# Kernel optimization log

Hardware: AMD Instinct MI355X
Metric: run time of the kernel (lower is better)

Reference implementation:

```python
import jax, jax.numpy as jnp
import numpy as np

B, S, H, M, E = 64, 512, 1024, 26, 676  # batch, seq, hidden, max_nodes, max_edges (M*M)


def setup_inputs() -> dict:
    key = jax.random.key(0)
    ks = jax.random.split(key, 16)
    seq = jax.random.normal(ks[0], (B, S, H), jnp.float32)
    # ragged, strictly-increasing sentence-end offsets in [1, S-1], zero-padded tail
    rng = np.random.RandomState(0)
    off = np.zeros((B, M - 1), np.int64)
    for b in range(B):
        c = rng.randint(5, M)  # count of valid offsets per sample (ragged)
        off[b, :c] = np.sort(rng.choice(np.arange(1, S), size=c, replace=False))
    s = 1.0 / np.sqrt(H)
    s3 = 1.0 / np.sqrt(3 * H)
    return {
        'sequence_outputs': seq,
        'proof_offsets': jnp.asarray(off),
        'node_labels': jax.random.randint(ks[1], (B, M), 0, 2),
        'edge_labels': jax.random.randint(ks[2], (B, E), 0, 2),
        'W_naf': jax.random.normal(ks[3], (H, H), jnp.float32) * s,
        'b_naf': jnp.zeros((H,), jnp.float32),
        'W_cd': jax.random.normal(ks[4], (H, H), jnp.float32) * s,
        'b_cd': jnp.zeros((H,), jnp.float32),
        'W_co': jax.random.normal(ks[5], (H, 2), jnp.float32) * s,
        'b_co': jnp.zeros((2,), jnp.float32),
        'W_nd': jax.random.normal(ks[6], (H, H), jnp.float32) * s,
        'b_nd': jnp.zeros((H,), jnp.float32),
        'W_no': jax.random.normal(ks[7], (H, 2), jnp.float32) * s,
        'b_no': jnp.zeros((2,), jnp.float32),
        'W_ed': jax.random.normal(ks[8], (3 * H, H), jnp.float32) * s3,
        'b_ed': jnp.zeros((H,), jnp.float32),
        'W_eo': jax.random.normal(ks[9], (H, 2), jnp.float32) * s,
        'b_eo': jnp.zeros((2,), jnp.float32),
    }


def reference(sequence_outputs, proof_offsets, node_labels, edge_labels,
              W_naf, b_naf, W_cd, b_cd, W_co, b_co,
              W_nd, b_nd, W_no, b_no, W_ed, b_ed, W_eo, b_eo):
    Bx, Sx, Hx = sequence_outputs.shape
    Mx = node_labels.shape[1]
    Ex = edge_labels.shape[1]

    cls = sequence_outputs[:, 0, :]                       # [B,H]
    naf = cls @ W_naf + b_naf                             # NAF node embedding
    logits = jnp.tanh(cls @ W_cd + b_cd) @ W_co + b_co    # RobertaClassificationHead (eval: dropout=id)

    # segment-mean pooling via inclusive prefix sums: segment j = tokens (prev_j, off_j]
    P = jnp.cumsum(sequence_outputs, axis=1)              # [B,S,H]
    off = proof_offsets                                   # [B,M-1]
    prev = jnp.concatenate([jnp.zeros((Bx, 1), off.dtype), off[:, :-1]], axis=1)
    valid = off > 0                                       # [B,M-1]
    seg_sum = (jnp.take_along_axis(P, off[..., None], axis=1)
               - jnp.take_along_axis(P, prev[..., None], axis=1))  # [B,M-1,H]
    seg_len = jnp.maximum(off - prev, 1).astype(sequence_outputs.dtype)
    seg_mean = seg_sum / seg_len[..., None] * valid[..., None]

    count = valid.sum(axis=1)                             # nodes per sample (excl. NAF)
    # node embeddings: seg means at 0..count-1, NAF at index count, zeros after
    node_full = jnp.concatenate([seg_mean, jnp.zeros((Bx, 1, Hx), seg_mean.dtype)], axis=1)  # [B,M,H]
    idx = jnp.arange(Mx)
    node_full = node_full + (idx[None, :, None] == count[:, None, None]) * naf[:, None, :]

    # all-pairs edge features over n=count+1 nodes, row-major flat k=i*n+j, zero-padded to E
    n = count + 1                                         # [B]
    k = jnp.arange(Ex)                                    # [E]
    i = jnp.clip(k[None, :] // n[:, None], 0, Mx - 1)     # [B,E]
    j = jnp.clip(k[None, :] % n[:, None], 0, Mx - 1)
    valid_e = (k[None, :] < (n * n)[:, None])[..., None]
    ni = jnp.take_along_axis(node_full, i[..., None], axis=1)  # [B,E,H]
    nj = jnp.take_along_axis(node_full, j[..., None], axis=1)
    edge = jnp.concatenate([nj, ni, nj - ni], axis=-1) * valid_e  # [B,E,3H]

    node_logits = jnp.tanh(node_full @ W_nd + b_nd) @ W_no + b_no
    edge_logits = jnp.tanh(edge @ W_ed + b_ed) @ W_eo + b_eo
    return (logits, node_logits, edge_logits)
```

## Files before the change

kernel.cpp:

```cpp
#include <hip/hip_runtime.h>
#include <hip/hip_bf16.h>

#define B_ 64
#define S_ 512
#define H_ 1024
#define M_ 26
#define E_ 676

typedef short bf16x8 __attribute__((ext_vector_type(8)));
typedef float f32x4 __attribute__((ext_vector_type(4)));

__device__ __forceinline__ void gload16(const void* g, void* l) {
    __builtin_amdgcn_global_load_lds((const __attribute__((address_space(1))) unsigned int*)g,
                                     (__attribute__((address_space(3))) unsigned int*)l,
                                     16, 0, 0);
}

__device__ __forceinline__ float tanh_fast(float x) {
    float e = __expf(2.0f * x);
    return 1.0f - 2.0f * __builtin_amdgcn_rcpf(e + 1.0f);
}

__global__ __launch_bounds__(256) void k_seg(
    const float* __restrict__ seq, const int* __restrict__ off,
    float* __restrict__ node_sum) {
    __shared__ float buf[4][16 * 256];
    __shared__ int offs_s[32];
    int bid = blockIdx.x;
    int tid = threadIdx.x;
    int b = bid >> 2, hs = bid & 3;
    int w = tid >> 6;
    int lane4 = (tid & 63) * 4;

    if (tid < M_ - 1) offs_s[tid] = off[b * (M_ - 1) + tid];
    __syncthreads();

    int c = 0;
    while (c < M_ - 1 && offs_s[c] > 0) c++;
    int offmax = offs_s[c - 1];
    int nt = (offmax + 15) >> 4;

    float* ns_base = node_sum + ((size_t)b * M_) * H_ + hs * 256 + tid;
    for (int m = c; m < M_; ++m) ns_base[(size_t)m * H_] = 0.f;

    const float* src0 = seq + (size_t)b * S_ * H_ + hs * 256;
#pragma unroll
    for (int j0 = 0; j0 < 4; ++j0) {
#pragma unroll
        for (int i = 0; i < 4; ++i) {
            int r = 4 * w + i;
            int t = 1 + 16 * j0 + r; t = min(t, 511);
            gload16(src0 + (size_t)t * H_ + lane4, &buf[j0][r * 256]);
        }
    }

    int m = 0;
    int cur = offs_s[0];
    float acc = 0.f;
    int ntc = (nt > 4) ? nt : 4;
    for (int j = 0; j < nt; ++j) {
        int ahead = ntc - 1 - j; ahead = (ahead > 3) ? 3 : ahead;
        if (ahead == 3)      asm volatile("s_waitcnt vmcnt(12)" ::: "memory");
        else if (ahead == 2) asm volatile("s_waitcnt vmcnt(8)" ::: "memory");
        else if (ahead == 1) asm volatile("s_waitcnt vmcnt(4)" ::: "memory");
        else                 asm volatile("s_waitcnt vmcnt(0)" ::: "memory");
        __builtin_amdgcn_s_barrier();

        const float* bj = &buf[j & 3][0];
        int tbase = 1 + 16 * j;
        if (tbase + 15 <= offmax) {
#pragma unroll
            for (int r = 0; r < 16; ++r) {
                int t = tbase + r;
                acc += bj[r * 256 + tid];
                if (t == cur) {
                    ns_base[(size_t)m * H_] = acc;
                    acc = 0.f; ++m;
                    cur = (m < c) ? offs_s[m] : 0x7fffffff;
                }
            }
        } else {
            for (int r = 0; r < 16; ++r) {
                int t = tbase + r;
                if (t > offmax) break;
                acc += bj[r * 256 + tid];
                if (t == cur) {
                    ns_base[(size_t)m * H_] = acc;
                    acc = 0.f; ++m;
                    cur = (m < c) ? offs_s[m] : 0x7fffffff;
                }
            }
        }
        __builtin_amdgcn_s_barrier();
        if (j + 4 < nt) {
#pragma unroll
            for (int i = 0; i < 4; ++i) {
                int r = 4 * w + i;
                int t = 1 + 16 * (j + 4) + r; t = min(t, 511);
                gload16(src0 + (size_t)t * H_ + lane4, &buf[j & 3][r * 256]);
            }
        }
    }
    asm volatile("s_waitcnt vmcnt(0)" ::: "memory");
}

__global__ __launch_bounds__(256) void k_stage1b(
    const float* __restrict__ seq, const int* __restrict__ off,
    const float* __restrict__ Wnaf, const float* __restrict__ Wcd,
    const float* __restrict__ Wnd, const float* __restrict__ Wed,
    const float* __restrict__ bed, const float* __restrict__ Weo,
    const float* __restrict__ beo,
    __hip_bfloat16* __restrict__ Wt, int* __restrict__ count,
    float* __restrict__ econ, float* __restrict__ naf, float* __restrict__ cdh) {
    __shared__ float smem[2048];
    int bid = blockIdx.x;
    int tid = threadIdx.x;

    if (bid < 256) {
        float (*As)[64] = (float(*)[64])smem;
        float (*Bs)[64] = (float(*)[64])(smem + 1024);
        int e = bid;
        int bx = e & 31;
        int kbase = (e >> 5) * 128;
        const float* W;
        float* dst;
        int cbase;
        if (bx < 16) { W = Wnaf; dst = naf; cbase = bx * 64; }
        else         { W = Wcd;  dst = cdh; cbase = (bx - 16) * 64; }
        int tx = tid % 16, ty = tid / 16;
        float c[4][4] = {};
        int la_row = tid / 4;
        int la_k4  = (tid % 4) * 4;
        int lb_k   = tid / 16;
        int lb_c4  = (tid % 16) * 4;
        for (int k0 = 0; k0 < 128; k0 += 16) {
            float4 a = *(const float4*)(seq + (size_t)la_row * S_ * H_ + kbase + k0 + la_k4);
            *(float4*)(&Bs[lb_k][lb_c4]) =
                *(const float4*)(W + (size_t)(kbase + k0 + lb_k) * H_ + cbase + lb_c4);
            As[la_k4 + 0][la_row] = a.x;
            As[la_k4 + 1][la_row] = a.y;
            As[la_k4 + 2][la_row] = a.z;
            As[la_k4 + 3][la_row] = a.w;
            __syncthreads();
#pragma unroll
            for (int kk = 0; kk < 16; ++kk) {
                float4 av = *(const float4*)(&As[kk][ty * 4]);
                float4 bv = *(const float4*)(&Bs[kk][tx * 4]);
                c[0][0] += av.x * bv.x; c[0][1] += av.x * bv.y; c[0][2] += av.x * bv.z; c[0][3] += av.x * bv.w;
                c[1][0] += av.y * bv.x; c[1][1] += av.y * bv.y; c[1][2] += av.y * bv.z; c[1][3] += av.y * bv.w;
                c[2][0] += av.z * bv.x; c[2][1] += av.z * bv.y; c[2][2] += av.z * bv.z; c[2][3] += av.z * bv.w;
                c[3][0] += av.w * bv.x; c[3][1] += av.w * bv.y; c[3][2] += av.w * bv.z; c[3][3] += av.w * bv.w;
            }
            __syncthreads();
        }
#pragma unroll
        for (int i = 0; i < 4; ++i)
#pragma unroll
            for (int j = 0; j < 4; ++j)
                atomicAdd(dst + (size_t)(ty * 4 + i) * H_ + cbase + tx * 4 + j, c[i][j]);
    } else if (bid < 3328) {
        float (*T)[33] = (float(*)[33])smem;
        int idx = bid - 256;
        int s = idx >> 10, rem = idx & 1023;
        int bx = rem & 31, by = rem >> 5;
        int c = tid & 31, r0 = tid >> 5;
        const int HH = H_ * H_;
#pragma unroll
        for (int i = 0; i < 4; ++i) {
            int r = r0 + 8 * i;
            size_t k = by * 32 + r, n = bx * 32 + c;
            float v;
            if (s == 0)      v = Wnd[k * H_ + n];
            else if (s == 1) v = Wed[k * H_ + n] + Wed[2 * HH + k * H_ + n];
            else             v = Wed[HH + k * H_ + n] - Wed[2 * HH + k * H_ + n];
            T[r][c] = v;
        }
        __syncthreads();
#pragma unroll
        for (int i = 0; i < 4; ++i) {
            int rr = r0 + 8 * i;
            Wt[(size_t)(s * H_ + bx * 32 + rr) * H_ + by * 32 + c] = __float2bfloat16(T[c][rr]);
        }
    } else if (bid == 3328) {
        if (tid < 64) {
            int b = tid;
            int c = 0;
            for (int m = 0; m < M_ - 1; ++m) c += (off[b * (M_ - 1) + m] > 0) ? 1 : 0;
            count[b] = c;
        }
    } else {
        float* s0 = smem; float* s1 = smem + 256;
        float a0 = 0.f, a1 = 0.f;
        for (int h = tid; h < H_; h += 256) {
            float t = tanh_fast(bed[h]);
            a0 += t * Weo[h * 2 + 0];
            a1 += t * Weo[h * 2 + 1];
        }
        s0[tid] = a0; s1[tid] = a1; __syncthreads();
        for (int o = 128; o > 0; o >>= 1) {
            if (tid < o) { s0[tid] += s0[tid + o]; s1[tid] += s1[tid + o]; }
            __syncthreads();
        }
        if (tid == 0) { econ[0] = s0[0] + beo[0]; econ[1] = s1[0] + beo[1]; }
    }
}

__global__ __launch_bounds__(256) void k_stage2(
    const float* __restrict__ sums, const int* __restrict__ off,
    const int* __restrict__ count, const float* __restrict__ naf,
    const float* __restrict__ bnaf, __hip_bfloat16* __restrict__ nodeB,
    const float* __restrict__ cdh, const float* __restrict__ bcd,
    const float* __restrict__ Wco, const float* __restrict__ bco,
    float* __restrict__ out) {
    __shared__ float smem[512];
    int bid = blockIdx.x;
    int tid = threadIdx.x;
    if (bid < 1664) {
        int b = bid / 26, m = bid - b * 26;
        int cnt = count[b];
        float4 v = make_float4(0, 0, 0, 0);
        const float4* row = (const float4*)(sums + ((size_t)(b * M_ + m)) * H_);
        if (m < M_ - 1) {
            int o = off[b * (M_ - 1) + m];
            if (o > 0) {
                int prev = (m > 0) ? off[b * (M_ - 1) + m - 1] : 0;
                float inv = 1.0f / (float)max(o - prev, 1);
                float4 s = row[tid];
                v = make_float4(s.x * inv, s.y * inv, s.z * inv, s.w * inv);
            }
        }
        if (m == cnt) {
            float4 a = ((const float4*)(naf + (size_t)b * H_))[tid];
            float4 bb = ((const float4*)bnaf)[tid];
            v.x += a.x + bb.x; v.y += a.y + bb.y; v.z += a.z + bb.z; v.w += a.w + bb.w;
        }
        __hip_bfloat16 __attribute__((aligned(8))) h[4] = {
            __float2bfloat16(v.x), __float2bfloat16(v.y),
            __float2bfloat16(v.z), __float2bfloat16(v.w)};
        *(ushort4*)(nodeB + ((size_t)(b * M_ + m)) * H_ + tid * 4) = *(const ushort4*)h;
    } else {
        int b = bid - 1664;
        float* s0 = smem; float* s1 = smem + 256;
        float a0 = 0.f, a1 = 0.f;
        for (int h = tid; h < H_; h += 256) {
            float t = tanh_fast(cdh[(size_t)b * H_ + h] + bcd[h]);
            a0 += t * Wco[h * 2 + 0];
            a1 += t * Wco[h * 2 + 1];
        }
        s0[tid] = a0; s1[tid] = a1; __syncthreads();
        for (int o = 128; o > 0; o >>= 1) {
            if (tid < o) { s0[tid] += s0[tid + o]; s1[tid] += s1[tid + o]; }
            __syncthreads();
        }
        if (tid == 0) { out[b * 2 + 0] = s0[0] + bco[0]; out[b * 2 + 1] = s1[0] + bco[1]; }
    }
}

#define GM 1664
#define GN 3072
#define GK 1024
__global__ __launch_bounds__(256) void k_mfma(const __hip_bfloat16* __restrict__ A,
                                              const __hip_bfloat16* __restrict__ Bt,
                                              float* __restrict__ C) {
    __shared__ __hip_bfloat16 As[128 * 32];
    __shared__ __hip_bfloat16 Bs[128 * 32];
    int tid = threadIdx.x;
    int wid = tid >> 6, ln = tid & 63;
    int row0 = blockIdx.y * 128, col0 = blockIdx.x * 128;
    const __hip_bfloat16* ga = A + (size_t)(row0 + wid * 16 + (ln >> 2)) * GK + (ln & 3) * 8;
    const __hip_bfloat16* gb = Bt + (size_t)(col0 + wid * 16 + (ln >> 2)) * GK + (ln & 3) * 8;
    __hip_bfloat16* lA = As + wid * 512;
    __hip_bfloat16* lB = Bs + wid * 512;
    int mrow = (wid >> 1) * 64, ncol = (wid & 1) * 64;
    int l15 = ln & 15, l4 = ln >> 4;
    f32x4 acc[4][4] = {};
    const __hip_bfloat16* pa = As + (size_t)(mrow + l15) * 32 + l4 * 8;
    const __hip_bfloat16* pb = Bs + (size_t)(ncol + l15) * 32 + l4 * 8;
    for (int k0 = 0; k0 < GK; k0 += 32) {
        gload16(ga, lA);
        gload16(ga + 64 * GK, lA + 2048);
        gload16(gb, lB);
        gload16(gb + 64 * GK, lB + 2048);
        ga += 32; gb += 32;
        __syncthreads();
        bf16x8 af[4], bf[4];
#pragma unroll
        for (int mi = 0; mi < 4; ++mi) af[mi] = *(const bf16x8*)(pa + mi * 16 * 32);
#pragma unroll
        for (int ni = 0; ni < 4; ++ni) bf[ni] = *(const bf16x8*)(pb + ni * 16 * 32);
#pragma unroll
        for (int mi = 0; mi < 4; ++mi)
#pragma unroll
            for (int ni = 0; ni < 4; ++ni)
                acc[mi][ni] = __builtin_amdgcn_mfma_f32_16x16x32_bf16(af[mi], bf[ni],
                                                                      acc[mi][ni], 0, 0, 0);
        __syncthreads();
    }
#pragma unroll
    for (int mi = 0; mi < 4; ++mi)
#pragma unroll
        for (int ni = 0; ni < 4; ++ni) {
            f32x4 v = acc[mi][ni];
            size_t r = row0 + mrow + mi * 16 + l4 * 4;
            size_t cc = col0 + ncol + ni * 16 + l15;
            C[(r + 0) * GN + cc] = v[0];
            C[(r + 1) * GN + cc] = v[1];
            C[(r + 2) * GN + cc] = v[2];
            C[(r + 3) * GN + cc] = v[3];
        }
}

__global__ __launch_bounds__(256) void k_stage4(
    const float* __restrict__ Cm, const int* __restrict__ count,
    const float* __restrict__ bnd, const float* __restrict__ Wno,
    const float* __restrict__ bno, const float* __restrict__ bed,
    const float* __restrict__ Weo, const float* __restrict__ beo,
    const float* __restrict__ econ, float* __restrict__ out_n,
    float* __restrict__ out_e) {
    int bid = blockIdx.x;
    int wid = threadIdx.x >> 6, lane = threadIdx.x & 63;
    if (bid < 416) {
        int r = bid * 4 + wid;
        const float4* src = (const float4*)(Cm + (size_t)r * GN);
        float a0 = 0.f, a1 = 0.f;
#pragma unroll
        for (int it = 0; it < 4; ++it) {
            int h = lane * 4 + it * 256;
            float4 s = src[lane + it * 64];
            float4 bb = *(const float4*)(bnd + h);
            float t0 = tanh_fast(s.x + bb.x), t1 = tanh_fast(s.y + bb.y);
            float t2 = tanh_fast(s.z + bb.z), t3 = tanh_fast(s.w + bb.w);
            a0 += t0 * Wno[h * 2 + 0] + t1 * Wno[h * 2 + 2] + t2 * Wno[h * 2 + 4] + t3 * Wno[h * 2 + 6];
            a1 += t0 * Wno[h * 2 + 1] + t1 * Wno[h * 2 + 3] + t2 * Wno[h * 2 + 5] + t3 * Wno[h * 2 + 7];
        }
        for (int o = 32; o > 0; o >>= 1) { a0 += __shfl_down(a0, o); a1 += __shfl_down(a1, o); }
        if (lane == 0) { out_n[(size_t)r * 2 + 0] = a0 + bno[0]; out_n[(size_t)r * 2 + 1] = a1 + bno[1]; }
    } else {
        int e = bid - 416;
        int b = e >> 4;
        int wg = (e & 15) * 4 + wid;
        int n = count[b] + 1;
        int n2 = n * n;
        float4 bed4[4], w04[4], w14[4];
#pragma unroll
        for (int it = 0; it < 4; ++it) {
            int h = lane * 4 + it * 256;
            bed4[it] = *(const float4*)(bed + h);
            w04[it] = make_float4(Weo[h * 2 + 0], Weo[h * 2 + 2], Weo[h * 2 + 4], Weo[h * 2 + 6]);
            w14[it] = make_float4(Weo[h * 2 + 1], Weo[h * 2 + 3], Weo[h * 2 + 5], Weo[h * 2 + 7]);
        }
        float e0 = econ[0], e1 = econ[1];
        float b0 = beo[0], b1 = beo[1];
        for (int k = wg; k < E_; k += 64) {
            float* dst = out_e + ((size_t)b * E_ + k) * 2;
            if (k >= n2) {
                if (lane == 0) { dst[0] = e0; dst[1] = e1; }
                continue;
            }
            int i = k / n, j = k - i * n;
            const float4* U4 = (const float4*)(Cm + (size_t)(b * M_ + j) * GN + H_);
            const float4* V4 = (const float4*)(Cm + (size_t)(b * M_ + i) * GN + 2 * H_);
            float a0 = 0.f, a1 = 0.f;
#pragma unroll
            for (int it = 0; it < 4; ++it) {
                float4 u = U4[lane + it * 64];
                float4 v = V4[lane + it * 64];
                float t0 = tanh_fast(u.x + v.x + bed4[it].x);
                float t1 = tanh_fast(u.y + v.y + bed4[it].y);
                float t2 = tanh_fast(u.z + v.z + bed4[it].z);
                float t3 = tanh_fast(u.w + v.w + bed4[it].w);
                a0 += t0 * w04[it].x + t1 * w04[it].y + t2 * w04[it].z + t3 * w04[it].w;
                a1 += t0 * w14[it].x + t1 * w14[it].y + t2 * w14[it].z + t3 * w14[it].w;
            }
            for (int o = 32; o > 0; o >>= 1) { a0 += __shfl_down(a0, o); a1 += __shfl_down(a1, o); }
            if (lane == 0) { dst[0] = a0 + b0; dst[1] = a1 + b1; }
        }
    }
}

extern "C" void kernel_launch(void* const* d_in, const int* in_sizes, int n_in,
                              void* d_out, int out_size, void* d_ws, size_t ws_size,
                              hipStream_t stream) {
    const float* seq  = (const float*)d_in[0];
    const int*   off  = (const int*)d_in[1];
    const float* Wnaf = (const float*)d_in[4];  const float* bnaf = (const float*)d_in[5];
    const float* Wcd  = (const float*)d_in[6];  const float* bcd  = (const float*)d_in[7];
    const float* Wco  = (const float*)d_in[8];  const float* bco  = (const float*)d_in[9];
    const float* Wnd  = (const float*)d_in[10]; const float* bnd  = (const float*)d_in[11];
    const float* Wno  = (const float*)d_in[12]; const float* bno  = (const float*)d_in[13];
    const float* Wed  = (const float*)d_in[14]; const float* bed  = (const float*)d_in[15];
    const float* Weo  = (const float*)d_in[16]; const float* beo  = (const float*)d_in[17];
    float* out = (float*)d_out;

    float* ws = (float*)d_ws;
    size_t p = 0;
    float* nodeS = ws + p;  p += (size_t)B_ * M_ * H_;
    float* naf   = ws + p;  p += (size_t)B_ * H_;
    float* cdh   = ws + p;  p += (size_t)B_ * H_;
    __hip_bfloat16* nodeB = (__hip_bfloat16*)(ws + p); p += (size_t)B_ * M_ * H_ / 2;
    __hip_bfloat16* Wt    = (__hip_bfloat16*)(ws + p); p += (size_t)3 * H_ * H_ / 2;
    float* Cbuf  = ws + p;  p += (size_t)B_ * M_ * 3 * H_;
    int*   cnt   = (int*)(ws + p); p += 64;
    float* econ  = ws + p;  p += 2;

    hipMemsetAsync(naf, 0, 2 * (size_t)B_ * H_ * sizeof(float), stream);

    k_seg<<<dim3(256), 256, 0, stream>>>(seq, off, nodeS);
    k_stage1b<<<dim3(3330), 256, 0, stream>>>(seq, off, Wnaf, Wcd, Wnd, Wed, bed, Weo, beo,
                                              Wt, cnt, econ, naf, cdh);
    k_stage2<<<dim3(1728), 256, 0, stream>>>(nodeS, off, cnt, naf, bnaf, nodeB,
                                             cdh, bcd, Wco, bco, out);
    k_mfma<<<dim3(GN / 128, GM / 128), 256, 0, stream>>>(nodeB, Wt, Cbuf);
    k_stage4<<<dim3(1440), 256, 0, stream>>>(Cbuf, cnt, bnd, Wno, bno, bed, Weo, beo, econ,
                                             out + B_ * 2, out + B_ * 2 + B_ * M_ * 2);
}
```

Measured before the change: 327.4 us.

## Fuse segment-mean bf16 output, node-head epilogue into GEMM, deepen prefetch

The segment-sum kernel now divides by segment length and writes bf16 node embeddings directly, so the fp32 node-sum buffer and most of the stage-2 normalization pass go away. The GEMM epilogue for the node-projection columns applies tanh and the 2-wide output projection in registers, reducing with shuffles and atomics, so only the edge columns of C are stored. The weight-transpose work is packed into fewer blocks that each process 12 tiles with software prefetch, and the sequence prefetch ring grows from 4 to 6 stages. This cuts global traffic and launch work, but adds atomics in the GEMM epilogue and uses more LDS in the segment kernel.

```diff
diff --git a/kernel.cpp b/kernel.cpp
--- a/kernel.cpp
+++ b/kernel.cpp
@@ -23,8 +23,8 @@
 
 __global__ __launch_bounds__(256) void k_seg(
     const float* __restrict__ seq, const int* __restrict__ off,
-    float* __restrict__ node_sum) {
-    __shared__ float buf[4][16 * 256];
+    __hip_bfloat16* __restrict__ nodeB) {
+    __shared__ float buf[6][16 * 256];
     __shared__ int offs_s[32];
     int bid = blockIdx.x;
     int tid = threadIdx.x;
@@ -39,69 +39,84 @@
     while (c < M_ - 1 && offs_s[c] > 0) c++;
     int offmax = offs_s[c - 1];
     int nt = (offmax + 15) >> 4;
-
-    float* ns_base = node_sum + ((size_t)b * M_) * H_ + hs * 256 + tid;
-    for (int m = c; m < M_; ++m) ns_base[(size_t)m * H_] = 0.f;
+    int ntc = (nt > 6) ? nt : 6;
+
+    __hip_bfloat16* nb = nodeB + ((size_t)b * M_) * H_ + hs * 256 + tid;
+    for (int m = c; m < M_; ++m) nb[(size_t)m * H_] = __float2bfloat16(0.f);
 
     const float* src0 = seq + (size_t)b * S_ * H_ + hs * 256;
 #pragma unroll
-    for (int j0 = 0; j0 < 4; ++j0) {
+    for (int j0 = 0; j0 < 6; ++j0)
 #pragma unroll
         for (int i = 0; i < 4; ++i) {
-            int r = 4 * w + i;
-            int t = 1 + 16 * j0 + r; t = min(t, 511);
-            gload16(src0 + (size_t)t * H_ + lane4, &buf[j0][r * 256]);
-        }
-    }
+            int t = 1 + 16 * j0 + 4 * w + i; t = min(t, 511);
+            gload16(src0 + (size_t)t * H_ + lane4, &buf[j0][(4 * w + i) * 256]);
+        }
 
     int m = 0;
     int cur = offs_s[0];
+    int prevoff = 0;
     float acc = 0.f;
-    int ntc = (nt > 4) ? nt : 4;
+    int slot = 0;
     for (int j = 0; j < nt; ++j) {
-        int ahead = ntc - 1 - j; ahead = (ahead > 3) ? 3 : ahead;
-        if (ahead == 3)      asm volatile("s_waitcnt vmcnt(12)" ::: "memory");
-        else if (ahead == 2) asm volatile("s_waitcnt vmcnt(8)" ::: "memory");
-        else if (ahead == 1) asm volatile("s_waitcnt vmcnt(4)" ::: "memory");
-        else                 asm volatile("s_waitcnt vmcnt(0)" ::: "memory");
+        int ahead = ntc - 1 - j; if (ahead > 5) ahead = 5;
+        switch (ahead) {
+            case 5:  asm volatile("s_waitcnt vmcnt(20)" ::: "memory"); break;
+            case 4:  asm volatile("s_waitcnt vmcnt(16)" ::: "memory"); break;
+            case 3:  asm volatile("s_waitcnt vmcnt(12)" ::: "memory"); break;
+            case 2:  asm volatile("s_waitcnt vmcnt(8)" ::: "memory"); break;
+            case 1:  asm volatile("s_waitcnt vmcnt(4)" ::: "memory"); break;
+            default: asm volatile("s_waitcnt vmcnt(0)" ::: "memory"); break;
+        }
         __builtin_amdgcn_s_barrier();
 
-        const float* bj = &buf[j & 3][0];
+        const float* bj = &buf[slot][0];
+        float vals[16];
+#pragma unroll
+        for (int r = 0; r < 16; ++r) vals[r] = bj[r * 256 + tid];
+
         int tbase = 1 + 16 * j;
-        if (tbase + 15 <= offmax) {
-#pragma unroll
-            for (int r = 0; r < 16; ++r) {
+        int rmax = offmax - tbase; if (rmax > 15) rmax = 15;
+#pragma unroll
+        for (int r = 0; r < 16; ++r) {
+            if (r <= rmax) {
+                acc += vals[r];
                 int t = tbase + r;
-                acc += bj[r * 256 + tid];
                 if (t == cur) {
-                    ns_base[(size_t)m * H_] = acc;
-                    acc = 0.f; ++m;
+                    float inv = 1.0f / (float)(cur - prevoff);
+                    nb[(size_t)m * H_] = __float2bfloat16(acc * inv);
+                    acc = 0.f; prevoff = cur; ++m;
                     cur = (m < c) ? offs_s[m] : 0x7fffffff;
                 }
             }
-        } else {
-            for (int r = 0; r < 16; ++r) {
-                int t = tbase + r;
-                if (t > offmax) break;
-                acc += bj[r * 256 + tid];
-                if (t == cur) {
-                    ns_base[(size_t)m * H_] = acc;
-                    acc = 0.f; ++m;
-                    cur = (m < c) ? offs_s[m] : 0x7fffffff;
-                }
-            }
         }
         __builtin_amdgcn_s_barrier();
-        if (j + 4 < nt) {
+        if (j + 6 < ntc) {
 #pragma unroll
             for (int i = 0; i < 4; ++i) {
-                int r = 4 * w + i;
-                int t = 1 + 16 * (j + 4) + r; t = min(t, 511);
-                gload16(src0 + (size_t)t * H_ + lane4, &buf[j & 3][r * 256]);
-            }
-        }
+                int t = 1 + 16 * (j + 6) + 4 * w + i; t = min(t, 511);
+                gload16(src0 + (size_t)t * H_ + lane4, &buf[slot][(4 * w + i) * 256]);
+            }
+        }
+        slot = (slot == 5) ? 0 : slot + 1;
     }
     asm volatile("s_waitcnt vmcnt(0)" ::: "memory");
+}
+
+__device__ __forceinline__ void load_tile(int idx, int c, int r0,
+                                          const float* __restrict__ Wnd,
+                                          const float* __restrict__ Wed, float* v) {
+    const int HH = H_ * H_;
+    int s = idx >> 10, rem = idx & 1023;
+    int bx = rem & 31, by = rem >> 5;
+#pragma unroll
+    for (int i = 0; i < 4; ++i) {
+        int r = r0 + 8 * i;
+        size_t k = (size_t)(by * 32 + r), n = (size_t)(bx * 32 + c);
+        if (s == 0)      v[i] = Wnd[k * H_ + n];
+        else if (s == 1) v[i] = Wed[k * H_ + n] + Wed[2 * HH + k * H_ + n];
+        else             v[i] = Wed[HH + k * H_ + n] - Wed[2 * HH + k * H_ + n];
+    }
 }
 
 __global__ __launch_bounds__(256) void k_stage1b(
@@ -119,9 +134,8 @@
     if (bid < 256) {
         float (*As)[64] = (float(*)[64])smem;
         float (*Bs)[64] = (float(*)[64])(smem + 1024);
-        int e = bid;
-        int bx = e & 31;
-        int kbase = (e >> 5) * 128;
+        int bx = bid & 31;
+        int kbase = (bid >> 5) * 128;
         const float* W;
         float* dst;
         int cbase;
@@ -158,30 +172,35 @@
 #pragma unroll
             for (int j = 0; j < 4; ++j)
                 atomicAdd(dst + (size_t)(ty * 4 + i) * H_ + cbase + tx * 4 + j, c[i][j]);
-    } else if (bid < 3328) {
+    } else if (bid < 512) {
         float (*T)[33] = (float(*)[33])smem;
-        int idx = bid - 256;
-        int s = idx >> 10, rem = idx & 1023;
-        int bx = rem & 31, by = rem >> 5;
         int c = tid & 31, r0 = tid >> 5;
-        const int HH = H_ * H_;
-#pragma unroll
-        for (int i = 0; i < 4; ++i) {
-            int r = r0 + 8 * i;
-            size_t k = by * 32 + r, n = bx * 32 + c;
-            float v;
-            if (s == 0)      v = Wnd[k * H_ + n];
-            else if (s == 1) v = Wed[k * H_ + n] + Wed[2 * HH + k * H_ + n];
-            else             v = Wed[HH + k * H_ + n] - Wed[2 * HH + k * H_ + n];
-            T[r][c] = v;
-        }
-        __syncthreads();
-#pragma unroll
-        for (int i = 0; i < 4; ++i) {
-            int rr = r0 + 8 * i;
-            Wt[(size_t)(s * H_ + bx * 32 + rr) * H_ + by * 32 + c] = __float2bfloat16(T[c][rr]);
-        }
-    } else if (bid == 3328) {
+        int base = (bid - 256) * 12;
+        float cur[4], nxt[4];
+        load_tile(base, c, r0, Wnd, Wed, cur);
+        for (int q = 0; q < 12; ++q) {
+            if (q < 11) load_tile(base + q + 1, c, r0, Wnd, Wed, nxt);
+            int idx = base + q;
+            int s = idx >> 10, rem = idx & 1023;
+            int bx = rem & 31, by = rem >> 5;
+#pragma unroll
+            for (int i = 0; i < 4; ++i) T[r0 + 8 * i][c] = cur[i];
+            asm volatile("s_waitcnt lgkmcnt(0)" ::: "memory");
+            __builtin_amdgcn_s_barrier();
+#pragma unroll
+            for (int i = 0; i < 4; ++i) {
+                int rr = r0 + 8 * i;
+                Wt[(size_t)(s * H_ + bx * 32 + rr) * H_ + by * 32 + c] =
+                    __float2bfloat16(T[c][rr]);
+            }
+            asm volatile("s_waitcnt lgkmcnt(0)" ::: "memory");
+            __builtin_amdgcn_s_barrier();
+            if (q < 11) {
+#pragma unroll
+                for (int i = 0; i < 4; ++i) cur[i] = nxt[i];
+            }
+        }
+    } else if (bid == 512) {
         if (tid < 64) {
             int b = tid;
             int c = 0;
@@ -205,41 +224,25 @@
     }
 }
 
-__global__ __launch_bounds__(256) void k_stage2(
-    const float* __restrict__ sums, const int* __restrict__ off,
-    const int* __restrict__ count, const float* __restrict__ naf,
-    const float* __restrict__ bnaf, __hip_bfloat16* __restrict__ nodeB,
+__global__ __launch_bounds__(256) void k_stage2s(
+    const float* __restrict__ naf, const float* __restrict__ bnaf,
+    const int* __restrict__ count, __hip_bfloat16* __restrict__ nodeB,
     const float* __restrict__ cdh, const float* __restrict__ bcd,
     const float* __restrict__ Wco, const float* __restrict__ bco,
     float* __restrict__ out) {
     __shared__ float smem[512];
     int bid = blockIdx.x;
     int tid = threadIdx.x;
-    if (bid < 1664) {
-        int b = bid / 26, m = bid - b * 26;
-        int cnt = count[b];
-        float4 v = make_float4(0, 0, 0, 0);
-        const float4* row = (const float4*)(sums + ((size_t)(b * M_ + m)) * H_);
-        if (m < M_ - 1) {
-            int o = off[b * (M_ - 1) + m];
-            if (o > 0) {
-                int prev = (m > 0) ? off[b * (M_ - 1) + m - 1] : 0;
-                float inv = 1.0f / (float)max(o - prev, 1);
-                float4 s = row[tid];
-                v = make_float4(s.x * inv, s.y * inv, s.z * inv, s.w * inv);
-            }
-        }
-        if (m == cnt) {
-            float4 a = ((const float4*)(naf + (size_t)b * H_))[tid];
-            float4 bb = ((const float4*)bnaf)[tid];
-            v.x += a.x + bb.x; v.y += a.y + bb.y; v.z += a.z + bb.z; v.w += a.w + bb.w;
-        }
+    if (bid < 64) {
+        int b = bid, cnt = count[b];
+        float4 a = ((const float4*)(naf + (size_t)b * H_))[tid];
+        float4 bb = ((const float4*)bnaf)[tid];
         __hip_bfloat16 __attribute__((aligned(8))) h[4] = {
-            __float2bfloat16(v.x), __float2bfloat16(v.y),
-            __float2bfloat16(v.z), __float2bfloat16(v.w)};
-        *(ushort4*)(nodeB + ((size_t)(b * M_ + m)) * H_ + tid * 4) = *(const ushort4*)h;
+            __float2bfloat16(a.x + bb.x), __float2bfloat16(a.y + bb.y),
+            __float2bfloat16(a.z + bb.z), __float2bfloat16(a.w + bb.w)};
+        *(ushort4*)(nodeB + ((size_t)(b * M_ + cnt)) * H_ + tid * 4) = *(const ushort4*)h;
     } else {
-        int b = bid - 1664;
+        int b = bid - 64;
         float* s0 = smem; float* s1 = smem + 256;
         float a0 = 0.f, a1 = 0.f;
         for (int h = tid; h < H_; h += 256) {
@@ -259,9 +262,13 @@
 #define GM 1664
 #define GN 3072
 #define GK 1024
+#define CB_N 2048
 __global__ __launch_bounds__(256) void k_mfma(const __hip_bfloat16* __restrict__ A,
                                               const __hip_bfloat16* __restrict__ Bt,
-                                              float* __restrict__ C) {
+                                              float* __restrict__ C,
+                                              const float* __restrict__ bnd,
+                                              const float* __restrict__ Wno,
+                                              float* __restrict__ nacc) {
     __shared__ __hip_bfloat16 As[128 * 32];
     __shared__ __hip_bfloat16 Bs[128 * 32];
     int tid = threadIdx.x;
@@ -296,49 +303,63 @@
                                                                       acc[mi][ni], 0, 0, 0);
         __syncthreads();
     }
-#pragma unroll
-    for (int mi = 0; mi < 4; ++mi)
+    if (col0 >= 1024) {
+#pragma unroll
+        for (int mi = 0; mi < 4; ++mi)
+#pragma unroll
+            for (int ni = 0; ni < 4; ++ni) {
+                f32x4 v = acc[mi][ni];
+                size_t r = row0 + mrow + mi * 16 + l4 * 4;
+                size_t cc = col0 + ncol + ni * 16 + l15 - 1024;
+                C[(r + 0) * CB_N + cc] = v[0];
+                C[(r + 1) * CB_N + cc] = v[1];
+                C[(r + 2) * CB_N + cc] = v[2];
+                C[(r + 3) * CB_N + cc] = v[3];
+            }
+    } else {
+        float bndv[4], w0v[4], w1v[4];
 #pragma unroll
         for (int ni = 0; ni < 4; ++ni) {
-            f32x4 v = acc[mi][ni];
-            size_t r = row0 + mrow + mi * 16 + l4 * 4;
-            size_t cc = col0 + ncol + ni * 16 + l15;
-            C[(r + 0) * GN + cc] = v[0];
-            C[(r + 1) * GN + cc] = v[1];
-            C[(r + 2) * GN + cc] = v[2];
-            C[(r + 3) * GN + cc] = v[3];
-        }
+            int col = col0 + ncol + ni * 16 + l15;
+            bndv[ni] = bnd[col];
+            w0v[ni] = Wno[2 * col];
+            w1v[ni] = Wno[2 * col + 1];
+        }
+#pragma unroll
+        for (int mi = 0; mi < 4; ++mi)
+#pragma unroll
+            for (int jj = 0; jj < 4; ++jj) {
+                float s0 = 0.f, s1 = 0.f;
+#pragma unroll
+                for (int ni = 0; ni < 4; ++ni) {
+                    float t = tanh_fast(acc[mi][ni][jj] + bndv[ni]);
+                    s0 += t * w0v[ni];
+                    s1 += t * w1v[ni];
+                }
+                s0 += __shfl_xor(s0, 1, 16); s0 += __shfl_xor(s0, 2, 16);
+                s0 += __shfl_xor(s0, 4, 16); s0 += __shfl_xor(s0, 8, 16);
+                s1 += __shfl_xor(s1, 1, 16); s1 += __shfl_xor(s1, 2, 16);
+                s1 += __shfl_xor(s1, 4, 16); s1 += __shfl_xor(s1, 8, 16);
+                if (l15 == 0) {
+                    int r = row0 + mrow + mi * 16 + l4 * 4 + jj;
+                    atomicAdd(nacc + 2 * r + 0, s0);
+                    atomicAdd(nacc + 2 * r + 1, s1);
+                }
+            }
+    }
 }
 
 __global__ __launch_bounds__(256) void k_stage4(
     const float* __restrict__ Cm, const int* __restrict__ count,
-    const float* __restrict__ bnd, const float* __restrict__ Wno,
-    const float* __restrict__ bno, const float* __restrict__ bed,
-    const float* __restrict__ Weo, const float* __restrict__ beo,
-    const float* __restrict__ econ, float* __restrict__ out_n,
-    float* __restrict__ out_e) {
+    const float* __restrict__ nacc, const float* __restrict__ bno,
+    const float* __restrict__ bed, const float* __restrict__ Weo,
+    const float* __restrict__ beo, const float* __restrict__ econ,
+    float* __restrict__ out_n, float* __restrict__ out_e) {
     int bid = blockIdx.x;
     int wid = threadIdx.x >> 6, lane = threadIdx.x & 63;
-    if (bid < 416) {
-        int r = bid * 4 + wid;
-        const float4* src = (const float4*)(Cm + (size_t)r * GN);
-        float a0 = 0.f, a1 = 0.f;
-#pragma unroll
-        for (int it = 0; it < 4; ++it) {
-            int h = lane * 4 + it * 256;
-            float4 s = src[lane + it * 64];
-            float4 bb = *(const float4*)(bnd + h);
-            float t0 = tanh_fast(s.x + bb.x), t1 = tanh_fast(s.y + bb.y);
-            float t2 = tanh_fast(s.z + bb.z), t3 = tanh_fast(s.w + bb.w);
-            a0 += t0 * Wno[h * 2 + 0] + t1 * Wno[h * 2 + 2] + t2 * Wno[h * 2 + 4] + t3 * Wno[h * 2 + 6];
-            a1 += t0 * Wno[h * 2 + 1] + t1 * Wno[h * 2 + 3] + t2 * Wno[h * 2 + 5] + t3 * Wno[h * 2 + 7];
-        }
-        for (int o = 32; o > 0; o >>= 1) { a0 += __shfl_down(a0, o); a1 += __shfl_down(a1, o); }
-        if (lane == 0) { out_n[(size_t)r * 2 + 0] = a0 + bno[0]; out_n[(size_t)r * 2 + 1] = a1 + bno[1]; }
-    } else {
-        int e = bid - 416;
-        int b = e >> 4;
-        int wg = (e & 15) * 4 + wid;
+    if (bid < 1024) {
+        int b = bid >> 4;
+        int wg = (bid & 15) * 4 + wid;
         int n = count[b] + 1;
         int n2 = n * n;
         float4 bed4[4], w04[4], w14[4];
@@ -358,8 +379,8 @@
                 continue;
             }
             int i = k / n, j = k - i * n;
-            const float4* U4 = (const float4*)(Cm + (size_t)(b * M_ + j) * GN + H_);
-            const float4* V4 = (const float4*)(Cm + (size_t)(b * M_ + i) * GN + 2 * H_);
+            const float4* U4 = (const float4*)(Cm + (size_t)(b * M_ + j) * CB_N);
+            const float4* V4 = (const float4*)(Cm + (size_t)(b * M_ + i) * CB_N + 1024);
             float a0 = 0.f, a1 = 0.f;
 #pragma unroll
             for (int it = 0; it < 4; ++it) {
@@ -375,6 +396,9 @@
             for (int o = 32; o > 0; o >>= 1) { a0 += __shfl_down(a0, o); a1 += __shfl_down(a1, o); }
             if (lane == 0) { dst[0] = a0 + b0; dst[1] = a1 + b1; }
         }
+    } else {
+        for (int idx = threadIdx.x; idx < GM * 2; idx += 256)
+            out_n[idx] = nacc[idx] + bno[idx & 1];
     }
 }
 
@@ -394,23 +418,23 @@
 
     float* ws = (float*)d_ws;
     size_t p = 0;
-    float* nodeS = ws + p;  p += (size_t)B_ * M_ * H_;
     float* naf   = ws + p;  p += (size_t)B_ * H_;
     float* cdh   = ws + p;  p += (size_t)B_ * H_;
+    float* nacc  = ws + p;  p += (size_t)GM * 2;
     __hip_bfloat16* nodeB = (__hip_bfloat16*)(ws + p); p += (size_t)B_ * M_ * H_ / 2;
     __hip_bfloat16* Wt    = (__hip_bfloat16*)(ws + p); p += (size_t)3 * H_ * H_ / 2;
-    float* Cbuf  = ws + p;  p += (size_t)B_ * M_ * 3 * H_;
+    float* Cbuf  = ws + p;  p += (size_t)GM * CB_N;
     int*   cnt   = (int*)(ws + p); p += 64;
     float* econ  = ws + p;  p += 2;
 
-    hipMemsetAsync(naf, 0, 2 * (size_t)B_ * H_ * sizeof(float), stream);
-
-    k_seg<<<dim3(256), 256, 0, stream>>>(seq, off, nodeS);
-    k_stage1b<<<dim3(3330), 256, 0, stream>>>(seq, off, Wnaf, Wcd, Wnd, Wed, bed, Weo, beo,
-                                              Wt, cnt, econ, naf, cdh);
-    k_stage2<<<dim3(1728), 256, 0, stream>>>(nodeS, off, cnt, naf, bnaf, nodeB,
+    hipMemsetAsync(naf, 0, (2 * (size_t)B_ * H_ + GM * 2) * sizeof(float), stream);
+
+    k_seg<<<dim3(256), 256, 0, stream>>>(seq, off, nodeB);
+    k_stage1b<<<dim3(514), 256, 0, stream>>>(seq, off, Wnaf, Wcd, Wnd, Wed, bed, Weo, beo,
+                                             Wt, cnt, econ, naf, cdh);
+    k_stage2s<<<dim3(128), 256, 0, stream>>>(naf, bnaf, cnt, nodeB,
                                              cdh, bcd, Wco, bco, out);
-    k_mfma<<<dim3(GN / 128, GM / 128), 256, 0, stream>>>(nodeB, Wt, Cbuf);
-    k_stage4<<<dim3(1440), 256, 0, stream>>>(Cbuf, cnt, bnd, Wno, bno, bed, Weo, beo, econ,
+    k_mfma<<<dim3(GN / 128, GM / 128), 256, 0, stream>>>(nodeB, Wt, Cbuf, bnd, Wno, nacc);
+    k_stage4<<<dim3(1025), 256, 0, stream>>>(Cbuf, cnt, nacc, bno, bed, Weo, beo, econ,
                                              out + B_ * 2, out + B_ * 2 + B_ * M_ * 2);
 }
```

Result: slower. 344.9 us (+5.3%).

## Compute segment means as bf16 MFMA selection-matrix matmul writing bf16 nodes directly

Applied to the files above, without the earlier changes.

Replaces the serial per-thread scan in the segment-sum kernel with a matmul: a 0/1 selection matrix in LDS times bf16-converted sequence tiles, computed with MFMA and scaled by each segment's inverse length. The result goes straight to bf16 node embeddings, so the fp32 node-sum buffer and most of stage2's per-node normalisation blocks go away. Stage2 now only writes the NAF row and computes the classifier head. The risk is that converting inputs to bf16 before summing loses precision, and the register-staged loads with a full vmcnt wait may expose memory latency.

```diff
diff --git a/kernel.cpp b/kernel.cpp
--- a/kernel.cpp
+++ b/kernel.cpp
@@ -21,87 +21,117 @@
     return 1.0f - 2.0f * __builtin_amdgcn_rcpf(e + 1.0f);
 }
 
-__global__ __launch_bounds__(256) void k_seg(
+__global__ __launch_bounds__(256) void k_segmm(
     const float* __restrict__ seq, const int* __restrict__ off,
-    float* __restrict__ node_sum) {
-    __shared__ float buf[4][16 * 256];
-    __shared__ int offs_s[32];
+    __hip_bfloat16* __restrict__ nodeB) {
+    __shared__ __hip_bfloat16 selL[32][520];
+    __shared__ __hip_bfloat16 ldsB[2][256][40];
+    __shared__ int offs_s[28];
+    __shared__ float invL[32];
+    int tid = threadIdx.x;
     int bid = blockIdx.x;
-    int tid = threadIdx.x;
-    int b = bid >> 2, hs = bid & 3;
-    int w = tid >> 6;
-    int lane4 = (tid & 63) * 4;
+    int b = bid >> 2, h0 = (bid & 3) * 256;
+    int w = tid >> 6, l = tid & 63;
 
     if (tid < M_ - 1) offs_s[tid] = off[b * (M_ - 1) + tid];
     __syncthreads();
-
     int c = 0;
     while (c < M_ - 1 && offs_s[c] > 0) c++;
     int offmax = offs_s[c - 1];
-    int nt = (offmax + 15) >> 4;
-
-    float* ns_base = node_sum + ((size_t)b * M_) * H_ + hs * 256 + tid;
-    for (int m = c; m < M_; ++m) ns_base[(size_t)m * H_] = 0.f;
-
-    const float* src0 = seq + (size_t)b * S_ * H_ + hs * 256;
-#pragma unroll
-    for (int j0 = 0; j0 < 4; ++j0) {
-#pragma unroll
-        for (int i = 0; i < 4; ++i) {
-            int r = 4 * w + i;
-            int t = 1 + 16 * j0 + r; t = min(t, 511);
-            gload16(src0 + (size_t)t * H_ + lane4, &buf[j0][r * 256]);
-        }
-    }
-
-    int m = 0;
-    int cur = offs_s[0];
-    float acc = 0.f;
-    int ntc = (nt > 4) ? nt : 4;
-    for (int j = 0; j < nt; ++j) {
-        int ahead = ntc - 1 - j; ahead = (ahead > 3) ? 3 : ahead;
-        if (ahead == 3)      asm volatile("s_waitcnt vmcnt(12)" ::: "memory");
-        else if (ahead == 2) asm volatile("s_waitcnt vmcnt(8)" ::: "memory");
-        else if (ahead == 1) asm volatile("s_waitcnt vmcnt(4)" ::: "memory");
-        else                 asm volatile("s_waitcnt vmcnt(0)" ::: "memory");
+
+    {
+        unsigned* p = (unsigned*)&selL[0][0];
+        const int tot = 32 * 520 * 2 / 4;
+        for (int i = tid; i < tot; i += 256) p[i] = 0u;
+    }
+    if (tid < 32)
+        invL[tid] = (tid < c) ? 1.0f / (float)(offs_s[tid] - (tid ? offs_s[tid - 1] : 0))
+                              : 0.0f;
+    __syncthreads();
+    for (int t = tid; t < 512; t += 256) {
+        if (t >= 1 && t <= offmax) {
+            int ms = 0;
+            while (ms < c && offs_s[ms] < t) ms++;
+            if (ms < c) *(unsigned short*)&selL[ms][t] = 0x3F80;
+        }
+    }
+    __syncthreads();
+
+    int nkt = (offmax >> 5) + 1;
+    const float* sb = seq + (size_t)b * S_ * H_ + h0;
+    float4 rg[8];
+#pragma unroll
+    for (int i = 0; i < 2; ++i)
+#pragma unroll
+        for (int r = 0; r < 4; ++r) {
+            int tl = (i * 4 + w) * 4 + r;
+            rg[i * 4 + r] = *(const float4*)(sb + (size_t)tl * H_ + 4 * l);
+        }
+    f32x4 acc[2][4] = {};
+
+    for (int kt = 0; kt < nkt; ++kt) {
+        asm volatile("s_waitcnt vmcnt(0)" ::: "memory");
+        ushort4 pk[2][4];
+#pragma unroll
+        for (int i = 0; i < 2; ++i)
+#pragma unroll
+            for (int q = 0; q < 4; ++q) {
+                float f0 = (q==0)?rg[i*4+0].x:(q==1)?rg[i*4+0].y:(q==2)?rg[i*4+0].z:rg[i*4+0].w;
+                float f1 = (q==0)?rg[i*4+1].x:(q==1)?rg[i*4+1].y:(q==2)?rg[i*4+1].z:rg[i*4+1].w;
+                float f2 = (q==0)?rg[i*4+2].x:(q==1)?rg[i*4+2].y:(q==2)?rg[i*4+2].z:rg[i*4+2].w;
+                float f3 = (q==0)?rg[i*4+3].x:(q==1)?rg[i*4+3].y:(q==2)?rg[i*4+3].z:rg[i*4+3].w;
+                __hip_bfloat16 __attribute__((aligned(8))) hh[4] = {
+                    __float2bfloat16(f0), __float2bfloat16(f1),
+                    __float2bfloat16(f2), __float2bfloat16(f3)};
+                pk[i][q] = *(const ushort4*)hh;
+            }
+        if (kt + 1 < nkt) {
+#pragma unroll
+            for (int i = 0; i < 2; ++i)
+#pragma unroll
+                for (int r = 0; r < 4; ++r) {
+                    int tl = (kt + 1) * 32 + (i * 4 + w) * 4 + r;
+                    rg[i * 4 + r] = *(const float4*)(sb + (size_t)tl * H_ + 4 * l);
+                }
+            __builtin_amdgcn_sched_barrier(0);
+        }
+#pragma unroll
+        for (int i = 0; i < 2; ++i)
+#pragma unroll
+            for (int q = 0; q < 4; ++q) {
+                int hl = 4 * l + q;
+                int tb = i * 4 + w;
+                *(ushort4*)&ldsB[kt & 1][hl][tb * 4] = pk[i][q];
+            }
+        asm volatile("s_waitcnt lgkmcnt(0)" ::: "memory");
         __builtin_amdgcn_s_barrier();
-
-        const float* bj = &buf[j & 3][0];
-        int tbase = 1 + 16 * j;
-        if (tbase + 15 <= offmax) {
-#pragma unroll
-            for (int r = 0; r < 16; ++r) {
-                int t = tbase + r;
-                acc += bj[r * 256 + tid];
-                if (t == cur) {
-                    ns_base[(size_t)m * H_] = acc;
-                    acc = 0.f; ++m;
-                    cur = (m < c) ? offs_s[m] : 0x7fffffff;
-                }
-            }
-        } else {
-            for (int r = 0; r < 16; ++r) {
-                int t = tbase + r;
-                if (t > offmax) break;
-                acc += bj[r * 256 + tid];
-                if (t == cur) {
-                    ns_base[(size_t)m * H_] = acc;
-                    acc = 0.f; ++m;
-                    cur = (m < c) ? offs_s[m] : 0x7fffffff;
-                }
-            }
-        }
-        __builtin_amdgcn_s_barrier();
-        if (j + 4 < nt) {
-#pragma unroll
-            for (int i = 0; i < 4; ++i) {
-                int r = 4 * w + i;
-                int t = 1 + 16 * (j + 4) + r; t = min(t, 511);
-                gload16(src0 + (size_t)t * H_ + lane4, &buf[j & 3][r * 256]);
-            }
-        }
-    }
-    asm volatile("s_waitcnt vmcnt(0)" ::: "memory");
+        int T0 = kt * 32;
+#pragma unroll
+        for (int mt = 0; mt < 2; ++mt) {
+            bf16x8 af = *(const bf16x8*)&selL[mt * 16 + (l & 15)][T0 + (l >> 4) * 8];
+#pragma unroll
+            for (int nn = 0; nn < 4; ++nn) {
+                bf16x8 bfr = *(const bf16x8*)&ldsB[kt & 1][(w * 4 + nn) * 16 + (l & 15)]
+                                                  [(l >> 4) * 8];
+                acc[mt][nn] = __builtin_amdgcn_mfma_f32_16x16x32_bf16(af, bfr,
+                                                                      acc[mt][nn], 0, 0, 0);
+            }
+        }
+    }
+#pragma unroll
+    for (int mt = 0; mt < 2; ++mt)
+#pragma unroll
+        for (int nn = 0; nn < 4; ++nn) {
+            f32x4 v = acc[mt][nn];
+            int hcol = h0 + (w * 4 + nn) * 16 + (l & 15);
+#pragma unroll
+            for (int r = 0; r < 4; ++r) {
+                int m = mt * 16 + (l >> 4) * 4 + r;
+                if (m < M_)
+                    nodeB[((size_t)(b * M_ + m)) * H_ + hcol] =
+                        __float2bfloat16(v[r] * invL[m]);
+            }
+        }
 }
 
 __global__ __launch_bounds__(256) void k_stage1b(
@@ -119,9 +149,8 @@
     if (bid < 256) {
         float (*As)[64] = (float(*)[64])smem;
         float (*Bs)[64] = (float(*)[64])(smem + 1024);
-        int e = bid;
-        int bx = e & 31;
-        int kbase = (e >> 5) * 128;
+        int bx = bid & 31;
+        int kbase = (bid >> 5) * 128;
         const float* W;
         float* dst;
         int cbase;
@@ -205,41 +234,25 @@
     }
 }
 
-__global__ __launch_bounds__(256) void k_stage2(
-    const float* __restrict__ sums, const int* __restrict__ off,
-    const int* __restrict__ count, const float* __restrict__ naf,
-    const float* __restrict__ bnaf, __hip_bfloat16* __restrict__ nodeB,
+__global__ __launch_bounds__(256) void k_stage2s(
+    const float* __restrict__ naf, const float* __restrict__ bnaf,
+    const int* __restrict__ count, __hip_bfloat16* __restrict__ nodeB,
     const float* __restrict__ cdh, const float* __restrict__ bcd,
     const float* __restrict__ Wco, const float* __restrict__ bco,
     float* __restrict__ out) {
     __shared__ float smem[512];
     int bid = blockIdx.x;
     int tid = threadIdx.x;
-    if (bid < 1664) {
-        int b = bid / 26, m = bid - b * 26;
-        int cnt = count[b];
-        float4 v = make_float4(0, 0, 0, 0);
-        const float4* row = (const float4*)(sums + ((size_t)(b * M_ + m)) * H_);
-        if (m < M_ - 1) {
-            int o = off[b * (M_ - 1) + m];
-            if (o > 0) {
-                int prev = (m > 0) ? off[b * (M_ - 1) + m - 1] : 0;
-                float inv = 1.0f / (float)max(o - prev, 1);
-                float4 s = row[tid];
-                v = make_float4(s.x * inv, s.y * inv, s.z * inv, s.w * inv);
-            }
-        }
-        if (m == cnt) {
-            float4 a = ((const float4*)(naf + (size_t)b * H_))[tid];
-            float4 bb = ((const float4*)bnaf)[tid];
-            v.x += a.x + bb.x; v.y += a.y + bb.y; v.z += a.z + bb.z; v.w += a.w + bb.w;
-        }
+    if (bid < 64) {
+        int b = bid, cnt = count[b];
+        float4 a = ((const float4*)(naf + (size_t)b * H_))[tid];
+        float4 bb = ((const float4*)bnaf)[tid];
         __hip_bfloat16 __attribute__((aligned(8))) h[4] = {
-            __float2bfloat16(v.x), __float2bfloat16(v.y),
-            __float2bfloat16(v.z), __float2bfloat16(v.w)};
-        *(ushort4*)(nodeB + ((size_t)(b * M_ + m)) * H_ + tid * 4) = *(const ushort4*)h;
+            __float2bfloat16(a.x + bb.x), __float2bfloat16(a.y + bb.y),
+            __float2bfloat16(a.z + bb.z), __float2bfloat16(a.w + bb.w)};
+        *(ushort4*)(nodeB + ((size_t)(b * M_ + cnt)) * H_ + tid * 4) = *(const ushort4*)h;
     } else {
-        int b = bid - 1664;
+        int b = bid - 64;
         float* s0 = smem; float* s1 = smem + 256;
         float a0 = 0.f, a1 = 0.f;
         for (int h = tid; h < H_; h += 256) {
@@ -394,21 +407,20 @@
 
     float* ws = (float*)d_ws;
     size_t p = 0;
-    float* nodeS = ws + p;  p += (size_t)B_ * M_ * H_;
     float* naf   = ws + p;  p += (size_t)B_ * H_;
     float* cdh   = ws + p;  p += (size_t)B_ * H_;
     __hip_bfloat16* nodeB = (__hip_bfloat16*)(ws + p); p += (size_t)B_ * M_ * H_ / 2;
     __hip_bfloat16* Wt    = (__hip_bfloat16*)(ws + p); p += (size_t)3 * H_ * H_ / 2;
-    float* Cbuf  = ws + p;  p += (size_t)B_ * M_ * 3 * H_;
+    float* Cbuf  = ws + p;  p += (size_t)GM * GN;
     int*   cnt   = (int*)(ws + p); p += 64;
     float* econ  = ws + p;  p += 2;
 
     hipMemsetAsync(naf, 0, 2 * (size_t)B_ * H_ * sizeof(float), stream);
 
-    k_seg<<<dim3(256), 256, 0, stream>>>(seq, off, nodeS);
+    k_segmm<<<dim3(256), 256, 0, stream>>>(seq, off, nodeB);
     k_stage1b<<<dim3(3330), 256, 0, stream>>>(seq, off, Wnaf, Wcd, Wnd, Wed, bed, Weo, beo,
                                               Wt, cnt, econ, naf, cdh);
-    k_stage2<<<dim3(1728), 256, 0, stream>>>(nodeS, off, cnt, naf, bnaf, nodeB,
+    k_stage2s<<<dim3(128), 256, 0, stream>>>(naf, bnaf, cnt, nodeB,
                                              cdh, bcd, Wco, bco, out);
     k_mfma<<<dim3(GN / 128, GM / 128), 256, 0, stream>>>(nodeB, Wt, Cbuf);
     k_stage4<<<dim3(1440), 256, 0, stream>>>(Cbuf, cnt, bnd, Wno, bno, bed, Weo, beo, econ,
```

Result: faster. 317.8 us (-2.9%).
